# Optimization experiments

Measured on AMD Instinct MI355X. Metric: run time of the kernel, lower is better.

The kernel has to match this reference:

```python
import jax, jax.numpy as jnp
import numpy as np

B, L, D = 2, 2048, 1024
H, HD = 16, 64   # num_heads, head_dim
LD = 256         # mla latent dim


def setup_inputs() -> dict:
    key = jax.random.key(0)
    ks = jax.random.split(key, 6)
    s = lambda fan_in: 1.0 / np.sqrt(fan_in)
    x_bld = jax.random.normal(ks[0], (B, L, D), dtype=jnp.float32)
    Wq = jax.random.normal(ks[1], (D, H, HD), dtype=jnp.float32) * s(D)
    Wkv_down = jax.random.normal(ks[2], (D, LD), dtype=jnp.float32) * s(D)
    Wk_up = jax.random.normal(ks[3], (LD, H, HD), dtype=jnp.float32) * s(LD)
    Wv_up = jax.random.normal(ks[4], (LD, H, HD), dtype=jnp.float32) * s(LD)
    Wout = jax.random.normal(ks[5], (H, HD, D), dtype=jnp.float32) * s(H * HD)
    return {"x_bld": x_bld, "Wq": Wq, "Wkv_down": Wkv_down,
            "Wk_up": Wk_up, "Wv_up": Wv_up, "Wout": Wout}


def reference(x_bld, Wq, Wkv_down, Wk_up, Wv_up, Wout):
    # projections
    q_blhd = jnp.einsum('bld,dhk->blhk', x_bld, Wq)
    latent_bll = jnp.einsum('bld,dc->blc', x_bld, Wkv_down)   # [B,L,LD]
    k_blhd = jnp.einsum('blc,chk->blhk', latent_bll, Wk_up)
    v_blhd = jnp.einsum('blc,chk->blhk', latent_bll, Wv_up)
    # attention scores [B,H,L,L]
    attn = jnp.einsum('bqhd,bkhd->bhqk', q_blhd, k_blhd) / jnp.sqrt(
        jnp.asarray(HD, dtype=x_bld.dtype))
    # causal mask (no window)
    l = x_bld.shape[1]
    mask = (jnp.arange(l)[None, :] <= jnp.arange(l)[:, None])[None, None]
    neg_inf = jnp.finfo(attn.dtype).min
    attn = jax.nn.softmax(jnp.where(mask, attn, neg_inf), axis=-1)
    y_blhd = jnp.einsum('bhqk,bkhd->bqhd', attn, v_blhd)
    return jnp.einsum('bqhd,hdo->bqo', y_blhd, Wout)
```

## Files before the change

### kernel.cpp

```cpp
#include <hip/hip_runtime.h>
#include <hip/hip_bf16.h>

#define BB   2
#define LL   2048
#define DD   1024
#define HH   16
#define HDD  64
#define LDIM 256
#define MTOT (BB * LL)

using short8  = __attribute__((ext_vector_type(8))) short;
using floatx4 = __attribute__((ext_vector_type(4))) float;

static __device__ __forceinline__ unsigned short f2bf(float x) {
  __hip_bfloat16 h = __float2bfloat16(x);
  return *reinterpret_cast<unsigned short*>(&h);
}
static __device__ __forceinline__ unsigned int pk_bf16(float a, float b) {
  return (unsigned int)f2bf(a) | ((unsigned int)f2bf(b) << 16);
}
static __device__ __forceinline__ void load_lds16(const unsigned short* g,
                                                  unsigned short* l) {
  __builtin_amdgcn_global_load_lds(
      (const __attribute__((address_space(1))) unsigned int*)g,
      (__attribute__((address_space(3))) unsigned int*)l, 16, 0, 0);
}
template <int N>
static __device__ __forceinline__ void waitcnt_vm() {
  if constexpr (N == 0) asm volatile("s_waitcnt vmcnt(0)" ::: "memory");
  else if constexpr (N == 3) asm volatile("s_waitcnt vmcnt(3)" ::: "memory");
  else if constexpr (N == 4) asm volatile("s_waitcnt vmcnt(4)" ::: "memory");
  else if constexpr (N == 8) asm volatile("s_waitcnt vmcnt(8)" ::: "memory");
}

__global__ __launch_bounds__(256) void cast_bf16(const float* __restrict__ in,
                                                 unsigned short* __restrict__ out,
                                                 int n4) {
  const int i = (blockIdx.x * 256 + threadIdx.x);
  if (i < n4) {
    float4 v = ((const float4*)in)[i];
    ushort4 o;
    o.x = f2bf(v.x); o.y = f2bf(v.y); o.z = f2bf(v.z); o.w = f2bf(v.w);
    ((ushort4*)out)[i] = o;
  }
}

__global__ __launch_bounds__(256) void transpose_cast5(
    const float* __restrict__ Wq, const float* __restrict__ Wkv,
    const float* __restrict__ Wku, const float* __restrict__ Wvu,
    const float* __restrict__ Wo,
    unsigned short* __restrict__ WqT, unsigned short* __restrict__ WkvT,
    unsigned short* __restrict__ WkuT, unsigned short* __restrict__ WvuT,
    unsigned short* __restrict__ WoT) {
  const float* src; unsigned short* dst; int R, C;
  switch (blockIdx.z) {
    case 0:  src = Wq;  dst = WqT;  R = 1024; C = 1024; break;
    case 1:  src = Wkv; dst = WkvT; R = 1024; C = 256;  break;
    case 2:  src = Wku; dst = WkuT; R = 256;  C = 1024; break;
    case 3:  src = Wvu; dst = WvuT; R = 256;  C = 1024; break;
    default: src = Wo;  dst = WoT;  R = 1024; C = 1024; break;
  }
  if ((int)blockIdx.x * 32 >= C || (int)blockIdx.y * 32 >= R) return;

  __shared__ float tile[32][33];
  const int tx = threadIdx.x, ty = threadIdx.y;
#pragma unroll
  for (int i = 0; i < 4; ++i) {
    const int r = blockIdx.y * 32 + ty + i * 8;
    tile[ty + i * 8][tx] = src[(size_t)r * C + blockIdx.x * 32 + tx];
  }
  __syncthreads();
#pragma unroll
  for (int i = 0; i < 4; ++i) {
    const int c = blockIdx.x * 32 + ty + i * 8;
    dst[(size_t)c * R + blockIdx.y * 32 + tx] = f2bf(tile[tx][ty + i * 8]);
  }
}

template <int KIND, int BMT, int BNT>
__global__ __launch_bounds__(256) void gemm2(const unsigned short* __restrict__ A,
                                             const unsigned short* __restrict__ Bt0,
                                             const unsigned short* __restrict__ Bt1,
                                             void* __restrict__ C0,
                                             void* __restrict__ C1,
                                             int M, int N, int K, int nsplit) {
  constexpr int IM = BMT / 32, JN = BNT / 32;
  constexpr int NLD = BMT / 64 + BNT / 64;
  __shared__ __align__(16) unsigned short As[2 * BMT * 32];
  __shared__ __align__(16) unsigned short Bs[2 * BNT * 32];

  const int tid  = threadIdx.x;
  const int w    = tid >> 6;
  const int lane = tid & 63;
  const int lo   = lane & 15;
  const int g    = lane >> 4;
  const int wr   = w >> 1, wc = w & 1;
  const int row0  = blockIdx.x * BMT;
  const int col0g = blockIdx.y * BNT;
  const bool second = (col0g >= nsplit);
  const unsigned short* Btp = second ? Bt1 : Bt0;
  const int col0 = second ? col0g - nsplit : col0g;

  floatx4 acc[IM][JN];
#pragma unroll
  for (int i = 0; i < IM; ++i)
#pragma unroll
    for (int j = 0; j < JN; ++j) acc[i][j] = (floatx4){0.f, 0.f, 0.f, 0.f};

  const int sr = tid >> 2;
  const int sc = tid & 3;

  auto stage = [&](int buf, int k0) {
#pragma unroll
    for (int inst = 0; inst < BMT / 64; ++inst) {
      const int r  = inst * 64 + sr;
      const int cs = sc ^ ((r >> 1) & 3);
      load_lds16(A + (size_t)(row0 + r) * K + k0 + cs * 8,
                 As + buf * (BMT * 32) + inst * 2048 + w * 512);
    }
#pragma unroll
    for (int inst = 0; inst < BNT / 64; ++inst) {
      const int r  = inst * 64 + sr;
      const int cs = sc ^ ((r >> 1) & 3);
      load_lds16(Btp + (size_t)(col0 + r) * K + k0 + cs * 8,
                 Bs + buf * (BNT * 32) + inst * 2048 + w * 512);
    }
  };

  const int nk = K / 32;
  stage(0, 0);
  for (int it = 0; it < nk; ++it) {
    const int cur = it & 1;
    if (it + 1 < nk) {
      stage(cur ^ 1, (it + 1) * 32);
      waitcnt_vm<NLD>();
    } else {
      waitcnt_vm<0>();
    }
    asm volatile("s_barrier" ::: "memory");

    const unsigned short* Ac = As + cur * (BMT * 32);
    const unsigned short* Bc = Bs + cur * (BNT * 32);
    short8 af[IM], bf[JN];
#pragma unroll
    for (int i = 0; i < IM; ++i) {
      const int rm = (BMT / 2) * wr + 16 * i + lo;
      af[i] = *(const short8*)(Ac + rm * 32 + ((g ^ ((rm >> 1) & 3)) * 8));
    }
#pragma unroll
    for (int j = 0; j < JN; ++j) {
      const int rn = (BNT / 2) * wc + 16 * j + lo;
      bf[j] = *(const short8*)(Bc + rn * 32 + ((g ^ ((rn >> 1) & 3)) * 8));
    }
#pragma unroll
    for (int i = 0; i < IM; ++i)
#pragma unroll
      for (int j = 0; j < JN; ++j)
        acc[i][j] = __builtin_amdgcn_mfma_f32_16x16x32_bf16(af[i], bf[j], acc[i][j], 0, 0, 0);

    asm volatile("s_barrier" ::: "memory");
  }

#pragma unroll
  for (int i = 0; i < IM; ++i) {
    const int mbase = row0 + (BMT / 2) * wr + 16 * i + g * 4;
#pragma unroll
    for (int j = 0; j < JN; ++j) {
      const int nl = col0 + (BNT / 2) * wc + 16 * j + lo;
      const int bq = mbase >> 11, hh = nl >> 6, d = nl & 63;
      if (KIND == 2 && second) {
        const int l = mbase & 2047;
        uint2 o;
        o.x = pk_bf16(acc[i][j][0], acc[i][j][1]);
        o.y = pk_bf16(acc[i][j][2], acc[i][j][3]);
        *(uint2*)(&((unsigned short*)C1)[((size_t)(bq * HH + hh) * HDD + d) * LL + l]) = o;
      } else {
#pragma unroll
        for (int r = 0; r < 4; ++r) {
          const float v = acc[i][j][r];
          const int mm = mbase + r;
          const int l = mm & 2047;
          if (KIND == 0) {
            ((float*)C0)[(size_t)mm * N + nl] = v;
          } else if (KIND == 1) {
            if (!second)
              ((unsigned short*)C0)[((size_t)(bq * HH + hh) * LL + l) * HDD + d] = f2bf(v);
            else
              ((unsigned short*)C1)[(size_t)mm * LDIM + nl] = f2bf(v);
          } else {
            ((unsigned short*)C0)[((size_t)(bq * HH + hh) * LL + l) * HDD + d] = f2bf(v);
          }
        }
      }
    }
  }
}

#define SC2 0.18033688011112042f

__global__ __launch_bounds__(256) void flash_mfma8(const unsigned short* __restrict__ Qh,
                                                   const unsigned short* __restrict__ Kh,
                                                   const unsigned short* __restrict__ Vt,
                                                   unsigned short* __restrict__ y) {
  const int w    = threadIdx.x >> 6;
  const int lane = threadIdx.x & 63;
  const int lo   = lane & 15;
  const int g    = lane >> 4;
  const int h    = blockIdx.x;
  const int b    = blockIdx.y;
  const int pair = blockIdx.z;
  const int qtH  = 31 - pair;
  const int qtL  = pair;

  __shared__ __align__(16) unsigned short Ks[3 * 64 * 64];
  __shared__ __align__(16) unsigned short Vs[3 * 64 * 64];
  __shared__ __align__(16) unsigned short Pq[4][16 * 64];

  const size_t bh = (size_t)(b * HH + h);
  const unsigned short* Qp = Qh + bh * LL * HDD;
  const unsigned short* Kp = Kh + bh * LL * HDD;
  const unsigned short* Vp = Vt + bh * (size_t)HDD * LL;
  unsigned short* Pw = Pq[w];

  const int qHw = qtH * 64 + w * 16;
  const int qLw = qtL * 64 + w * 16;

  short8 qfH0 = *(const short8*)(Qp + (size_t)(qHw + lo) * HDD + g * 8);
  short8 qfH1 = *(const short8*)(Qp + (size_t)(qHw + lo) * HDD + 32 + g * 8);
  short8 qfL0 = *(const short8*)(Qp + (size_t)(qLw + lo) * HDD + g * 8);
  short8 qfL1 = *(const short8*)(Qp + (size_t)(qLw + lo) * HDD + 32 + g * 8);

  floatx4 otH[4], otL[4];
#pragma unroll
  for (int ds = 0; ds < 4; ++ds) {
    otH[ds] = (floatx4){0.f, 0.f, 0.f, 0.f};
    otL[ds] = (floatx4){0.f, 0.f, 0.f, 0.f};
  }
  float lsumH = 0.f, lsumL = 0.f;

  const int srow = lane >> 3;
  const int sch  = lane & 7;

  auto stage = [&](int buf, int k0) {
#pragma unroll
    for (int t = 0; t < 2; ++t) {
      const int rbase = w * 16 + t * 8;
      const int row   = rbase + srow;
      const int cs    = sch ^ (row & 7);
      load_lds16(Kp + (size_t)(k0 + row) * HDD + cs * 8, Ks + buf * 4096 + rbase * 64);
      load_lds16(Vp + (size_t)row * LL + k0 + cs * 8,    Vs + buf * 4096 + rbase * 64);
    }
  };

  auto tile_qt = [&](const unsigned short* Kc, const unsigned short* Vc,
                     short8 qf0, short8 qf1, floatx4* ot, float& lsum,
                     int qw, int k0, bool masked) {
    floatx4 st[4];
#pragma unroll
    for (int ks = 0; ks < 4; ++ks) {
      const int rm = ks * 16 + lo;
      short8 a0 = *(const short8*)(Kc + rm * 64 + ((g ^ (rm & 7)) * 8));
      short8 a1 = *(const short8*)(Kc + rm * 64 + (((4 + g) ^ (rm & 7)) * 8));
      floatx4 s = (floatx4){0.f, 0.f, 0.f, 0.f};
      s = __builtin_amdgcn_mfma_f32_16x16x32_bf16(a0, qf0, s, 0, 0, 0);
      s = __builtin_amdgcn_mfma_f32_16x16x32_bf16(a1, qf1, s, 0, 0, 0);
      st[ks] = s;
    }
    if (!masked) {
#pragma unroll
      for (int ks = 0; ks < 4; ++ks) {
        float p[4];
#pragma unroll
        for (int r = 0; r < 4; ++r) {
          p[r] = __builtin_amdgcn_exp2f(st[ks][r] * SC2);
          lsum += p[r];
        }
        uint2 w2;
        w2.x = pk_bf16(p[0], p[1]);
        w2.y = pk_bf16(p[2], p[3]);
        *(uint2*)(Pw + lo * 64 + (((ks * 2 + (g >> 1)) ^ (lo & 7)) * 8) + (g & 1) * 4) = w2;
      }
    } else {
      const int qq = qw + lo;
#pragma unroll
      for (int ks = 0; ks < 4; ++ks) {
        float p[4];
#pragma unroll
        for (int r = 0; r < 4; ++r) {
          const int kk = k0 + ks * 16 + g * 4 + r;
          const float e = __builtin_amdgcn_exp2f(st[ks][r] * SC2);
          p[r] = (kk <= qq) ? e : 0.f;
          lsum += p[r];
        }
        uint2 w2;
        w2.x = pk_bf16(p[0], p[1]);
        w2.y = pk_bf16(p[2], p[3]);
        *(uint2*)(Pw + lo * 64 + (((ks * 2 + (g >> 1)) ^ (lo & 7)) * 8) + (g & 1) * 4) = w2;
      }
    }
    short8 pf0 = *(const short8*)(Pw + lo * 64 + ((g ^ (lo & 7)) * 8));
    short8 pf1 = *(const short8*)(Pw + lo * 64 + (((4 + g) ^ (lo & 7)) * 8));
#pragma unroll
    for (int ds = 0; ds < 4; ++ds) {
      const int rm = ds * 16 + lo;
      short8 v0 = *(const short8*)(Vc + rm * 64 + ((g ^ (rm & 7)) * 8));
      short8 v1 = *(const short8*)(Vc + rm * 64 + (((4 + g) ^ (rm & 7)) * 8));
      ot[ds] = __builtin_amdgcn_mfma_f32_16x16x32_bf16(v0, pf0, ot[ds], 0, 0, 0);
      ot[ds] = __builtin_amdgcn_mfma_f32_16x16x32_bf16(v1, pf1, ot[ds], 0, 0, 0);
    }
  };

  const int ntiles = qtH + 1;
  stage(0, 0);
  stage(1, 64);
  for (int it = 0; it < ntiles; ++it) {
    const int cur = it % 3;
    const int k0  = it * 64;
    if (it + 2 < ntiles) {
      stage((it + 2) % 3, k0 + 128);
      waitcnt_vm<8>();
    } else if (it + 1 < ntiles) {
      waitcnt_vm<4>();
    } else {
      waitcnt_vm<0>();
    }
    asm volatile("s_barrier" ::: "memory");

    const unsigned short* Kc = Ks + cur * 4096;
    const unsigned short* Vc = Vs + cur * 4096;

    tile_qt(Kc, Vc, qfH0, qfH1, otH, lsumH, qHw, k0, it == qtH);
    if (it <= qtL)
      tile_qt(Kc, Vc, qfL0, qfL1, otL, lsumL, qLw, k0, it == qtL);

    asm volatile("s_barrier" ::: "memory");
  }

  auto finish = [&](floatx4* ot, float lsum, int qw) {
    float s = lsum;
    s += __shfl_xor(s, 16);
    s += __shfl_xor(s, 32);
    const float inv = 1.0f / s;
#pragma unroll
    for (int ds = 0; ds < 4; ++ds) {
      uint2 o;
      o.x = pk_bf16(ot[ds][0] * inv, ot[ds][1] * inv);
      o.y = pk_bf16(ot[ds][2] * inv, ot[ds][3] * inv);
      *(uint2*)(y + (size_t)(b * LL + qw + lo) * (HH * HDD) + h * HDD + ds * 16 + g * 4) = o;
    }
  };
  finish(otH, lsumH, qHw);
  finish(otL, lsumL, qLw);
}

extern "C" void kernel_launch(void* const* d_in, const int* in_sizes, int n_in,
                              void* d_out, int out_size, void* d_ws, size_t ws_size,
                              hipStream_t stream) {
  const float* x   = (const float*)d_in[0];
  const float* Wq  = (const float*)d_in[1];
  const float* Wkv = (const float*)d_in[2];
  const float* Wku = (const float*)d_in[3];
  const float* Wvu = (const float*)d_in[4];
  const float* Wo  = (const float*)d_in[5];
  float* out = (float*)d_out;

  unsigned short* xb     = (unsigned short*)d_ws;
  unsigned short* WqT    = xb + (size_t)MTOT * DD;
  unsigned short* WkvT   = WqT + 1024 * 1024;
  unsigned short* WkuT   = WkvT + 256 * 1024;
  unsigned short* WvuT   = WkuT + 1024 * 256;
  unsigned short* WoT    = WvuT + 1024 * 256;
  unsigned short* latent = WoT + 1024 * 1024;
  unsigned short* Qh     = latent + (size_t)MTOT * LDIM;
  unsigned short* Kh     = Qh + (size_t)MTOT * DD;
  unsigned short* Vt     = Kh + (size_t)MTOT * DD;
  unsigned short* y      = Vt + (size_t)MTOT * DD;

  cast_bf16<<<dim3(MTOT * DD / 1024), dim3(256), 0, stream>>>(x, xb, MTOT * DD / 4);
  transpose_cast5<<<dim3(32, 32, 5), dim3(32, 8), 0, stream>>>(
      Wq, Wkv, Wku, Wvu, Wo, WqT, WkvT, WkuT, WvuT, WoT);

  gemm2<1, 128, 64><<<dim3(MTOT / 128, 1280 / 64), dim3(256), 0, stream>>>(
      xb, WqT, WkvT, Qh, latent, MTOT, 1280, DD, 1024);
  gemm2<2, 128, 128><<<dim3(MTOT / 128, 2048 / 128), dim3(256), 0, stream>>>(
      latent, WkuT, WvuT, Kh, Vt, MTOT, 2048, LDIM, 1024);

  flash_mfma8<<<dim3(HH, BB, 16), dim3(256), 0, stream>>>(Qh, Kh, Vt, y);

  gemm2<0, 128, 64><<<dim3(MTOT / 128, DD / 64), dim3(256), 0, stream>>>(
      y, WoT, nullptr, out, nullptr, MTOT, DD, DD, DD);
}
```

Baseline: 170.3 us.

## Use BK=64 tiles in projection GEMMs and interleave two q-tiles in flash attention

The GEMM kernel gains a K-tile template parameter. The Q/latent and output projections now stage 64-wide K slices with an 8-way XOR swizzle, halving the number of barrier and wait rounds per K sweep. The flash kernel splits per-tile work into separate QK, softmax and PV phases, and it interleaves the high and low q-tile of each block using separate P buffers, which gives the scheduler more independent MFMA and LDS work to overlap. Barriers now also drain LDS counters. The cost is more LDS use and register pressure from holding two sets of score tiles at once.

```diff
diff --git a/kernel.cpp b/kernel.cpp
--- a/kernel.cpp
+++ b/kernel.cpp
@@ -28,9 +28,12 @@
 template <int N>
 static __device__ __forceinline__ void waitcnt_vm() {
   if constexpr (N == 0) asm volatile("s_waitcnt vmcnt(0)" ::: "memory");
-  else if constexpr (N == 3) asm volatile("s_waitcnt vmcnt(3)" ::: "memory");
   else if constexpr (N == 4) asm volatile("s_waitcnt vmcnt(4)" ::: "memory");
+  else if constexpr (N == 6) asm volatile("s_waitcnt vmcnt(6)" ::: "memory");
   else if constexpr (N == 8) asm volatile("s_waitcnt vmcnt(8)" ::: "memory");
+}
+static __device__ __forceinline__ void lds_drain_barrier() {
+  asm volatile("s_waitcnt lgkmcnt(0)\n\ts_barrier" ::: "memory");
 }
 
 __global__ __launch_bounds__(256) void cast_bf16(const float* __restrict__ in,
@@ -77,7 +80,7 @@
   }
 }
 
-template <int KIND, int BMT, int BNT>
+template <int KIND, int BMT, int BNT, int BKT>
 __global__ __launch_bounds__(256) void gemm2(const unsigned short* __restrict__ A,
                                              const unsigned short* __restrict__ Bt0,
                                              const unsigned short* __restrict__ Bt1,
@@ -85,9 +88,12 @@
                                              void* __restrict__ C1,
                                              int M, int N, int K, int nsplit) {
   constexpr int IM = BMT / 32, JN = BNT / 32;
-  constexpr int NLD = BMT / 64 + BNT / 64;
-  __shared__ __align__(16) unsigned short As[2 * BMT * 32];
-  __shared__ __align__(16) unsigned short Bs[2 * BNT * 32];
+  constexpr int TA = BMT * BKT, TB = BNT * BKT;
+  constexpr int NIA = TA / 2048, NIB = TB / 2048;
+  constexpr int NLD = NIA + NIB;
+  constexpr int RPI = 2048 / BKT;
+  __shared__ __align__(16) unsigned short As[2 * TA];
+  __shared__ __align__(16) unsigned short Bs[2 * TB];
 
   const int tid  = threadIdx.x;
   const int w    = tid >> 6;
@@ -107,58 +113,66 @@
 #pragma unroll
     for (int j = 0; j < JN; ++j) acc[i][j] = (floatx4){0.f, 0.f, 0.f, 0.f};
 
-  const int sr = tid >> 2;
-  const int sc = tid & 3;
+  const int sr = (BKT == 32) ? (tid >> 2) : (tid >> 3);
+  const int sc = (BKT == 32) ? (tid & 3) : (tid & 7);
+
+  auto swz = [](int chunk, int row) {
+    if constexpr (BKT == 32) return chunk ^ ((row >> 1) & 3);
+    else                     return chunk ^ (row & 7);
+  };
 
   auto stage = [&](int buf, int k0) {
 #pragma unroll
-    for (int inst = 0; inst < BMT / 64; ++inst) {
-      const int r  = inst * 64 + sr;
-      const int cs = sc ^ ((r >> 1) & 3);
+    for (int inst = 0; inst < NIA; ++inst) {
+      const int r  = inst * RPI + sr;
+      const int cs = swz(sc, r);
       load_lds16(A + (size_t)(row0 + r) * K + k0 + cs * 8,
-                 As + buf * (BMT * 32) + inst * 2048 + w * 512);
-    }
-#pragma unroll
-    for (int inst = 0; inst < BNT / 64; ++inst) {
-      const int r  = inst * 64 + sr;
-      const int cs = sc ^ ((r >> 1) & 3);
+                 As + buf * TA + inst * 2048 + w * 512);
+    }
+#pragma unroll
+    for (int inst = 0; inst < NIB; ++inst) {
+      const int r  = inst * RPI + sr;
+      const int cs = swz(sc, r);
       load_lds16(Btp + (size_t)(col0 + r) * K + k0 + cs * 8,
-                 Bs + buf * (BNT * 32) + inst * 2048 + w * 512);
-    }
-  };
-
-  const int nk = K / 32;
+                 Bs + buf * TB + inst * 2048 + w * 512);
+    }
+  };
+
+  const int nk = K / BKT;
   stage(0, 0);
   for (int it = 0; it < nk; ++it) {
     const int cur = it & 1;
     if (it + 1 < nk) {
-      stage(cur ^ 1, (it + 1) * 32);
+      stage(cur ^ 1, (it + 1) * BKT);
       waitcnt_vm<NLD>();
     } else {
       waitcnt_vm<0>();
     }
     asm volatile("s_barrier" ::: "memory");
 
-    const unsigned short* Ac = As + cur * (BMT * 32);
-    const unsigned short* Bc = Bs + cur * (BNT * 32);
-    short8 af[IM], bf[JN];
-#pragma unroll
-    for (int i = 0; i < IM; ++i) {
-      const int rm = (BMT / 2) * wr + 16 * i + lo;
-      af[i] = *(const short8*)(Ac + rm * 32 + ((g ^ ((rm >> 1) & 3)) * 8));
-    }
-#pragma unroll
-    for (int j = 0; j < JN; ++j) {
-      const int rn = (BNT / 2) * wc + 16 * j + lo;
-      bf[j] = *(const short8*)(Bc + rn * 32 + ((g ^ ((rn >> 1) & 3)) * 8));
-    }
-#pragma unroll
-    for (int i = 0; i < IM; ++i)
-#pragma unroll
-      for (int j = 0; j < JN; ++j)
-        acc[i][j] = __builtin_amdgcn_mfma_f32_16x16x32_bf16(af[i], bf[j], acc[i][j], 0, 0, 0);
-
-    asm volatile("s_barrier" ::: "memory");
+    const unsigned short* Ac = As + cur * TA;
+    const unsigned short* Bc = Bs + cur * TB;
+#pragma unroll
+    for (int kk = 0; kk < BKT / 32; ++kk) {
+      short8 af[IM], bf[JN];
+#pragma unroll
+      for (int i = 0; i < IM; ++i) {
+        const int rm = (BMT / 2) * wr + 16 * i + lo;
+        af[i] = *(const short8*)(Ac + (size_t)rm * BKT + swz(kk * 4 + g, rm) * 8);
+      }
+#pragma unroll
+      for (int j = 0; j < JN; ++j) {
+        const int rn = (BNT / 2) * wc + 16 * j + lo;
+        bf[j] = *(const short8*)(Bc + (size_t)rn * BKT + swz(kk * 4 + g, rn) * 8);
+      }
+#pragma unroll
+      for (int i = 0; i < IM; ++i)
+#pragma unroll
+        for (int j = 0; j < JN; ++j)
+          acc[i][j] = __builtin_amdgcn_mfma_f32_16x16x32_bf16(af[i], bf[j], acc[i][j], 0, 0, 0);
+    }
+
+    lds_drain_barrier();
   }
 
 #pragma unroll
@@ -198,7 +212,7 @@
 
 #define SC2 0.18033688011112042f
 
-__global__ __launch_bounds__(256) void flash_mfma8(const unsigned short* __restrict__ Qh,
+__global__ __launch_bounds__(256) void flash_mfma9(const unsigned short* __restrict__ Qh,
                                                    const unsigned short* __restrict__ Kh,
                                                    const unsigned short* __restrict__ Vt,
                                                    unsigned short* __restrict__ y) {
@@ -214,13 +228,14 @@
 
   __shared__ __align__(16) unsigned short Ks[3 * 64 * 64];
   __shared__ __align__(16) unsigned short Vs[3 * 64 * 64];
-  __shared__ __align__(16) unsigned short Pq[4][16 * 64];
+  __shared__ __align__(16) unsigned short Pq[4][2][16 * 64];
 
   const size_t bh = (size_t)(b * HH + h);
   const unsigned short* Qp = Qh + bh * LL * HDD;
   const unsigned short* Kp = Kh + bh * LL * HDD;
   const unsigned short* Vp = Vt + bh * (size_t)HDD * LL;
-  unsigned short* Pw = Pq[w];
+  unsigned short* PwH = Pq[w][0];
+  unsigned short* PwL = Pq[w][1];
 
   const int qHw = qtH * 64 + w * 16;
   const int qLw = qtL * 64 + w * 16;
@@ -252,20 +267,20 @@
     }
   };
 
-  auto tile_qt = [&](const unsigned short* Kc, const unsigned short* Vc,
-                     short8 qf0, short8 qf1, floatx4* ot, float& lsum,
-                     int qw, int k0, bool masked) {
-    floatx4 st[4];
+  auto qk = [&](const unsigned short* Kc, short8 q0f, short8 q1f, floatx4* st) {
 #pragma unroll
     for (int ks = 0; ks < 4; ++ks) {
       const int rm = ks * 16 + lo;
       short8 a0 = *(const short8*)(Kc + rm * 64 + ((g ^ (rm & 7)) * 8));
       short8 a1 = *(const short8*)(Kc + rm * 64 + (((4 + g) ^ (rm & 7)) * 8));
       floatx4 s = (floatx4){0.f, 0.f, 0.f, 0.f};
-      s = __builtin_amdgcn_mfma_f32_16x16x32_bf16(a0, qf0, s, 0, 0, 0);
-      s = __builtin_amdgcn_mfma_f32_16x16x32_bf16(a1, qf1, s, 0, 0, 0);
+      s = __builtin_amdgcn_mfma_f32_16x16x32_bf16(a0, q0f, s, 0, 0, 0);
+      s = __builtin_amdgcn_mfma_f32_16x16x32_bf16(a1, q1f, s, 0, 0, 0);
       st[ks] = s;
     }
+  };
+  auto sm = [&](floatx4* st, unsigned short* P, float& lsum, int qw, int k0,
+                bool masked) {
     if (!masked) {
 #pragma unroll
       for (int ks = 0; ks < 4; ++ks) {
@@ -278,7 +293,7 @@
         uint2 w2;
         w2.x = pk_bf16(p[0], p[1]);
         w2.y = pk_bf16(p[2], p[3]);
-        *(uint2*)(Pw + lo * 64 + (((ks * 2 + (g >> 1)) ^ (lo & 7)) * 8) + (g & 1) * 4) = w2;
+        *(uint2*)(P + lo * 64 + (((ks * 2 + (g >> 1)) ^ (lo & 7)) * 8) + (g & 1) * 4) = w2;
       }
     } else {
       const int qq = qw + lo;
@@ -295,11 +310,13 @@
         uint2 w2;
         w2.x = pk_bf16(p[0], p[1]);
         w2.y = pk_bf16(p[2], p[3]);
-        *(uint2*)(Pw + lo * 64 + (((ks * 2 + (g >> 1)) ^ (lo & 7)) * 8) + (g & 1) * 4) = w2;
+        *(uint2*)(P + lo * 64 + (((ks * 2 + (g >> 1)) ^ (lo & 7)) * 8) + (g & 1) * 4) = w2;
       }
     }
-    short8 pf0 = *(const short8*)(Pw + lo * 64 + ((g ^ (lo & 7)) * 8));
-    short8 pf1 = *(const short8*)(Pw + lo * 64 + (((4 + g) ^ (lo & 7)) * 8));
+  };
+  auto pv = [&](const unsigned short* Vc, const unsigned short* P, floatx4* ot) {
+    short8 pf0 = *(const short8*)(P + lo * 64 + ((g ^ (lo & 7)) * 8));
+    short8 pf1 = *(const short8*)(P + lo * 64 + (((4 + g) ^ (lo & 7)) * 8));
 #pragma unroll
     for (int ds = 0; ds < 4; ++ds) {
       const int rm = ds * 16 + lo;
@@ -328,12 +345,17 @@
 
     const unsigned short* Kc = Ks + cur * 4096;
     const unsigned short* Vc = Vs + cur * 4096;
-
-    tile_qt(Kc, Vc, qfH0, qfH1, otH, lsumH, qHw, k0, it == qtH);
-    if (it <= qtL)
-      tile_qt(Kc, Vc, qfL0, qfL1, otL, lsumL, qLw, k0, it == qtL);
-
-    asm volatile("s_barrier" ::: "memory");
+    const bool doL = (it <= qtL);
+
+    floatx4 stH[4], stL[4];
+    qk(Kc, qfH0, qfH1, stH);
+    if (doL) qk(Kc, qfL0, qfL1, stL);
+    sm(stH, PwH, lsumH, qHw, k0, it == qtH);
+    if (doL) sm(stL, PwL, lsumL, qLw, k0, it == qtL);
+    pv(Vc, PwH, otH);
+    if (doL) pv(Vc, PwL, otL);
+
+    lds_drain_barrier();
   }
 
   auto finish = [&](floatx4* ot, float lsum, int qw) {
@@ -380,13 +402,13 @@
   transpose_cast5<<<dim3(32, 32, 5), dim3(32, 8), 0, stream>>>(
       Wq, Wkv, Wku, Wvu, Wo, WqT, WkvT, WkuT, WvuT, WoT);
 
-  gemm2<1, 128, 64><<<dim3(MTOT / 128, 1280 / 64), dim3(256), 0, stream>>>(
+  gemm2<1, 128, 64, 64><<<dim3(MTOT / 128, 1280 / 64), dim3(256), 0, stream>>>(
       xb, WqT, WkvT, Qh, latent, MTOT, 1280, DD, 1024);
-  gemm2<2, 128, 128><<<dim3(MTOT / 128, 2048 / 128), dim3(256), 0, stream>>>(
+  gemm2<2, 128, 128, 32><<<dim3(MTOT / 128, 2048 / 128), dim3(256), 0, stream>>>(
       latent, WkuT, WvuT, Kh, Vt, MTOT, 2048, LDIM, 1024);
 
-  flash_mfma8<<<dim3(HH, BB, 16), dim3(256), 0, stream>>>(Qh, Kh, Vt, y);
-
-  gemm2<0, 128, 64><<<dim3(MTOT / 128, DD / 64), dim3(256), 0, stream>>>(
+  flash_mfma9<<<dim3(HH, BB, 16), dim3(256), 0, stream>>>(Qh, Kh, Vt, y);
+
+  gemm2<0, 128, 64, 64><<<dim3(MTOT / 128, DD / 64), dim3(256), 0, stream>>>(
       y, WoT, nullptr, out, nullptr, MTOT, DD, DD, DD);
 }
```

Result: no change. 167.2 us (-1.8%).
